# Performance work log

Hardware: AMD Instinct MI355X
Metric: run time of the kernel (lower is better)

The kernel has to match this reference:

```python
import jax, jax.numpy as jnp
import numpy as np

HID = 256; NH = 8; DH = 32; NL = 2
NV = 20000; NT = 50000; NE = 100000; NC = 8; FIN = 64


def setup_inputs() -> dict:
    ks = jax.random.split(jax.random.key(0), 32)
    f = lambda i, sh, s: jax.random.normal(ks[i], sh, dtype=jnp.float32) * s
    return {
        "x_v": f(0, (NV, FIN), 1.0),
        "x_t": f(1, (NT, FIN), 1.0),
        "ei_vt_src": jax.random.randint(ks[2], (NE,), 0, NV),
        "ei_vt_dst": jax.random.randint(ks[3], (NE,), 0, NT),
        "ei_tv_src": jax.random.randint(ks[4], (NE,), 0, NT),
        "ei_tv_dst": jax.random.randint(ks[5], (NE,), 0, NV),
        "ei_tt_src": jax.random.randint(ks[6], (NE,), 0, NT),
        "ei_tt_dst": jax.random.randint(ks[7], (NE,), 0, NT),
        "current": jax.random.randint(ks[8], (NC, 2), 0, NV),
        "W_in_v": f(9, (FIN, HID), 0.05), "b_in_v": jnp.zeros((HID,)),
        "W_in_t": f(10, (FIN, HID), 0.05), "b_in_t": jnp.zeros((HID,)),
        "Wk": f(11, (NL, 2, HID, HID), 0.05), "bk": jnp.zeros((NL, 2, HID)),
        "Wq": f(12, (NL, 2, HID, HID), 0.05), "bq": jnp.zeros((NL, 2, HID)),
        "Wv": f(13, (NL, 2, HID, HID), 0.05), "bv": jnp.zeros((NL, 2, HID)),
        "Wa": f(14, (NL, 2, HID, HID), 0.05), "ba": jnp.zeros((NL, 2, HID)),
        "skip": jnp.zeros((NL, 2)),
        "a_rel": f(15, (NL, 3, NH, DH, DH), 0.1),
        "m_rel": f(16, (NL, 3, NH, DH, DH), 0.1),
        "p_rel": jnp.ones((NL, 3, NH)),
        "Ws1": f(17, (2 * HID, HID), 0.05), "bs1": jnp.zeros((HID,)),
        "Ws2": f(18, (HID, 2), 0.05), "bs2": jnp.zeros((2,)),
    }


def reference(x_v, x_t, ei_vt_src, ei_vt_dst, ei_tv_src, ei_tv_dst,
              ei_tt_src, ei_tt_dst, current,
              W_in_v, b_in_v, W_in_t, b_in_t,
              Wk, bk, Wq, bq, Wv, bv, Wa, ba, skip,
              a_rel, m_rel, p_rel, Ws1, bs1, Ws2, bs2):
    scale = 1.0 / jnp.sqrt(jnp.float32(DH))
    # input projections + relu (lin_dict)
    hv = jax.nn.relu(x_v @ W_in_v + b_in_v)
    ht = jax.nn.relu(x_t @ W_in_t + b_in_t)
    # edge types: (src_type, dst_type, rel_idx, src_idx, dst_idx); 0=vehicle, 1=track
    edges = [(0, 1, 0, ei_vt_src, ei_vt_dst),
             (1, 0, 1, ei_tv_src, ei_tv_dst),
             (1, 1, 2, ei_tt_src, ei_tt_dst)]
    for l in range(NL):
        h = (hv, ht)
        proj = lambda W, b, t: (h[t] @ W[l, t] + b[l, t]).reshape(-1, NH, DH)
        k = (proj(Wk, bk, 0), proj(Wk, bk, 1))
        q = (proj(Wq, bq, 0), proj(Wq, bq, 1))
        v = (proj(Wv, bv, 0), proj(Wv, bv, 1))
        agg = [jnp.zeros((NV, NH, DH), jnp.float32),
               jnp.zeros((NT, NH, DH), jnp.float32)]
        for (st, dt, r, si, di) in edges:
            nd = agg[dt].shape[0]
            ke = jnp.einsum('ehd,hdf->ehf', k[st][si], a_rel[l, r])  # [E,H,D]
            ve = jnp.einsum('ehd,hdf->ehf', v[st][si], m_rel[l, r])  # [E,H,D]
            logit = (q[dt][di] * ke).sum(-1) * p_rel[l, r] * scale    # [E,H]
            m = jax.ops.segment_max(logit, di, num_segments=nd)
            e = jnp.exp(logit - m[di])
            s = jax.ops.segment_sum(e, di, num_segments=nd)
            alpha = e / (s[di] + 1e-16)
            agg[dt] = agg[dt] + jax.ops.segment_sum(alpha[..., None] * ve, di,
                                                    num_segments=nd)
        new = []
        for t in (0, 1):
            o = jax.nn.gelu(agg[t].reshape(-1, HID), approximate=False) @ Wa[l, t] + ba[l, t]
            beta = jax.nn.sigmoid(skip[l, t])
            new.append(beta * o + (1.0 - beta) * h[t])
        hv, ht = new
    # batched Scorer over (current vehicles) x (all tracks); cat([track, vehicle])
    veh = hv[current[:, 0]]                 # [C,HID]
    tpart = ht @ Ws1[:HID]                  # [NT,HID]
    vpart = veh @ Ws1[HID:] + bs1           # [C,HID]
    hmid = jax.nn.relu(tpart[None, :, :] + vpart[:, None, :])  # [C,NT,HID]
    out = hmid @ Ws2 + bs2                  # [C,NT,2]
    return out[..., 0], jax.nn.sigmoid(out[..., 1])
```

## Files before the change

### kernel.cpp

```cpp
#include <hip/hip_runtime.h>
#include <hip/hip_bf16.h>
#include <math.h>

#define HID 256
#define NH 8
#define DH 32
#define NL 2
#define NV 20000
#define NT 50000
#define NE 100000
#define NC 8
#define FIN 64

typedef unsigned short u16;
typedef unsigned int u32;
typedef short s16x8 __attribute__((ext_vector_type(8)));
typedef float f32x4 __attribute__((ext_vector_type(4)));

__device__ __forceinline__ float bf2f(u16 u) { return __uint_as_float(((u32)u) << 16); }
__device__ __forceinline__ u16 f2bf(float f) {
    u32 x = __float_as_uint(f);
    u32 r = ((x >> 16) & 1u) + 0x7fffu;
    return (u16)((x + r) >> 16);
}
__device__ __forceinline__ void up2(u32 u, float& a, float& b) {
    a = __uint_as_float(u << 16);
    b = __uint_as_float(u & 0xffff0000u);
}
__device__ __forceinline__ s16x8 gelu8(s16x8 a) {
    s16x8 r;
#pragma unroll
    for (int i = 0; i < 8; i++) {
        float v = bf2f((u16)a[i]);
        v = 0.5f * v * (1.f + erff(v * 0.70710678118654752f));
        r[i] = (short)f2bf(v);
    }
    return r;
}

__global__ void k_zero_i(int* __restrict__ p, int n) {
    for (int i = blockIdx.x * 256 + threadIdx.x; i < n; i += gridDim.x * 256) p[i] = 0;
}

__global__ void k_hist3(const int* __restrict__ d0, const int* __restrict__ d1, const int* __restrict__ d2,
                        int* __restrict__ cnt3) {
    int r = blockIdx.x >> 9;
    int b = blockIdx.x & 511;
    const int* dst = (r == 0) ? d0 : (r == 1) ? d1 : d2;
    int* cnt = cnt3 + (size_t)r * NT;
    for (int e = b * 256 + threadIdx.x; e < NE; e += 512 * 256)
        atomicAdd(&cnt[dst[e]], 1);
}

__global__ __launch_bounds__(1024) void k_scan3(const int* __restrict__ cnt3,
                                                int* __restrict__ rp0, int* __restrict__ rp1, int* __restrict__ rp2) {
    int r = blockIdx.x;
    const int* cnt = cnt3 + (size_t)r * NT;
    int* rp = (r == 0) ? rp0 : (r == 1) ? rp1 : rp2;
    int n = (r == 1) ? NV : NT;
    __shared__ int wsum[16];
    __shared__ int carry_s;
    int t = threadIdx.x, lane = t & 63, wv = t >> 6;
    if (t == 0) { carry_s = 0; rp[0] = 0; }
    __syncthreads();
    for (int base = 0; base < n; base += 1024) {
        int v = (base + t < n) ? cnt[base + t] : 0;
        int x = v;
#pragma unroll
        for (int off = 1; off < 64; off <<= 1) {
            int y = __shfl_up(x, off, 64);
            if (lane >= off) x += y;
        }
        if (lane == 63) wsum[wv] = x;
        __syncthreads();
        if (wv == 0 && lane < 16) {
            int s = wsum[lane];
#pragma unroll
            for (int off = 1; off < 16; off <<= 1) {
                int y = __shfl_up(s, off, 64);
                if (lane >= off) s += y;
            }
            wsum[lane] = s;
        }
        __syncthreads();
        int prefix = carry_s + (wv > 0 ? wsum[wv - 1] : 0);
        if (base + t < n) rp[base + t + 1] = prefix + x;
        __syncthreads();
        if (t == 0) carry_s += wsum[15];
        __syncthreads();
    }
}

__global__ void k_copy3(const int* __restrict__ rp0, const int* __restrict__ rp1, const int* __restrict__ rp2,
                        int* __restrict__ fill3) {
    int r = blockIdx.x >> 8;
    int b = blockIdx.x & 255;
    const int* rp = (r == 0) ? rp0 : (r == 1) ? rp1 : rp2;
    int n = (r == 1) ? NV : NT;
    int* fill = fill3 + (size_t)r * NT;
    for (int i = b * 256 + threadIdx.x; i < n; i += 256 * 256) fill[i] = rp[i];
}

__global__ void k_scatter3(const int* __restrict__ d0, const int* __restrict__ s0,
                           const int* __restrict__ d1, const int* __restrict__ s1,
                           const int* __restrict__ d2, const int* __restrict__ s2,
                           int* __restrict__ fill3,
                           int* __restrict__ es0, int* __restrict__ es1, int* __restrict__ es2) {
    int r = blockIdx.x >> 9;
    int b = blockIdx.x & 511;
    const int* dst = (r == 0) ? d0 : (r == 1) ? d1 : d2;
    const int* src = (r == 0) ? s0 : (r == 1) ? s1 : s2;
    int* fill = fill3 + (size_t)r * NT;
    int* es = (r == 0) ? es0 : (r == 1) ? es1 : es2;
    for (int e = b * 256 + threadIdx.x; e < NE; e += 512 * 256) {
        int d = dst[e];
        int p = atomicAdd(&fill[d], 1);
        es[p] = src[e];
    }
}

__global__ __launch_bounds__(256) void k_in_proj(const float* __restrict__ X, const float* __restrict__ W,
                          const float* __restrict__ b, u16* __restrict__ Y, int N) {
    const int NPB = 16;
    __shared__ float xs[NPB][FIN];
    int n0 = blockIdx.x * NPB;
    int t = threadIdx.x;
    for (int idx = t; idx < NPB * FIN; idx += 256) {
        int i = idx >> 6, c = idx & 63;
        int n = n0 + i;
        xs[i][c] = (n < N) ? X[(size_t)n * FIN + c] : 0.f;
    }
    __syncthreads();
    float acc[NPB];
#pragma unroll
    for (int i = 0; i < NPB; i++) acc[i] = 0.f;
    for (int c = 0; c < FIN; c++) {
        float w = W[c * HID + t];
#pragma unroll
        for (int i = 0; i < NPB; i++) acc[i] += xs[i][c] * w;
    }
    float bb = b[t];
    for (int i = 0; i < NPB; i++) {
        int n = n0 + i;
        if (n < N) Y[(size_t)n * HID + t] = f2bf(fmaxf(acc[i] + bb, 0.f));
    }
}

__device__ __forceinline__ int swz_idx(int k, int n) {
    int ks = k >> 5, r = k & 31;
    int j = r & 7;
    int l = ((r >> 3) << 4) | (n & 15);
    int nt = n >> 4;
    return ((ks * 16 + nt) * 64 + l) * 8 + j;
}

__global__ __launch_bounds__(256) void k_fuse_w(const float* __restrict__ W, const float* __restrict__ b,
                        const float* __restrict__ R, u16* __restrict__ Wsw, float* __restrict__ bout) {
    int h = blockIdx.x;
    __shared__ float sR[DH * DH];
    int t = threadIdx.x;
    for (int idx = t; idx < DH * DH; idx += 256) sR[idx] = R[h * DH * DH + idx];
    __syncthreads();
    int f = t & 31, c0 = t >> 5;
    for (int c = c0; c < HID; c += 8) {
        float acc = 0.f;
#pragma unroll
        for (int d = 0; d < DH; d++) acc += W[c * HID + h * DH + d] * sR[d * DH + f];
        Wsw[swz_idx(c, h * DH + f)] = f2bf(acc);
    }
    if (t < DH) {
        float acc = 0.f;
#pragma unroll
        for (int d = 0; d < DH; d++) acc += b[h * DH + d] * sR[d * DH + t];
        bout[h * DH + t] = acc;
    }
}

__global__ __launch_bounds__(256) void k_swz_multi(const float* __restrict__ Wq, const float* __restrict__ Wa,
                                                   const float* __restrict__ Ws1, u16* __restrict__ out) {
    int slot = blockIdx.x >> 8;
    int idx = ((blockIdx.x & 255) << 8) | threadIdx.x;
    const float* src = (slot < 4) ? (Wq + (size_t)slot * 65536)
                     : (slot < 8) ? (Wa + (size_t)(slot - 4) * 65536)
                                  : Ws1;
    int j = idx & 7, l = (idx >> 3) & 63, nt = (idx >> 9) & 15, ks = idx >> 13;
    int k = ks * 32 + (l >> 4) * 8 + j;
    int n = nt * 16 + (l & 15);
    out[(size_t)slot * 65536 + idx] = f2bf(src[k * HID + n]);
}

template <int MODE, int GELU>
__global__ __launch_bounds__(256) void k_mm(const u16* __restrict__ X, const u16* __restrict__ Wsw,
                                            const float* __restrict__ bias, void* __restrict__ Y,
                                            const float* __restrict__ skip_, int N) {
    int tid = threadIdx.x;
    int w = tid >> 6, lane = tid & 63;
    int r0 = blockIdx.x * 16;
    int rA = r0 + (lane & 15);
    int koffg = lane >> 4;
    s16x8 a[8];
    if (rA < N) {
        const s16x8* ap = (const s16x8*)(X + (size_t)rA * HID) + koffg;
#pragma unroll
        for (int ks = 0; ks < 8; ks++) a[ks] = ap[ks * 4];
    } else {
#pragma unroll
        for (int ks = 0; ks < 8; ks++) a[ks] = (s16x8){0, 0, 0, 0, 0, 0, 0, 0};
    }
    if (GELU) {
#pragma unroll
        for (int ks = 0; ks < 8; ks++) a[ks] = gelu8(a[ks]);
    }
    f32x4 acc[4];
#pragma unroll
    for (int nt = 0; nt < 4; nt++) acc[nt] = (f32x4){0.f, 0.f, 0.f, 0.f};
    const s16x8* wp = (const s16x8*)Wsw;
#pragma unroll
    for (int ks = 0; ks < 8; ks++) {
        const s16x8* wq = wp + (size_t)ks * 16 * 64 + lane;
#pragma unroll
        for (int nt = 0; nt < 4; nt++) {
            s16x8 b = wq[(w * 4 + nt) * 64];
            acc[nt] = __builtin_amdgcn_mfma_f32_16x16x32_bf16(a[ks], b, acc[nt], 0, 0, 0);
        }
    }
    int colb = lane & 15;
    int rowb = r0 + koffg * 4;
    float beta = 0.f, ombeta = 0.f;
    if (MODE == 2) { beta = 1.f / (1.f + expf(-skip_[0])); ombeta = 1.f - beta; }
#pragma unroll
    for (int nt = 0; nt < 4; nt++) {
        int col = w * 64 + nt * 16 + colb;
        float bb = (MODE == 1 || MODE == 3) ? 0.f : bias[col];
#pragma unroll
        for (int j = 0; j < 4; j++) {
            int row = rowb + j;
            if (row < N) {
                float v = acc[nt][j] + bb;
                if (MODE == 0 || MODE == 3) {
                    ((u16*)Y)[(size_t)row * HID + col] = f2bf(v);
                } else if (MODE == 1) {
                    ((float*)Y)[(size_t)row * HID + col] = v;
                } else {
                    u16* hp = (u16*)Y + (size_t)row * HID + col;
                    *hp = f2bf(beta * v + ombeta * bf2f(*hp));
                }
            }
        }
    }
}

__global__ __launch_bounds__(256) void k_mm2(const u16* __restrict__ X,
                                             const u16* __restrict__ W1, const float* __restrict__ b1, u16* __restrict__ Y1,
                                             const u16* __restrict__ W2, const float* __restrict__ b2, u16* __restrict__ Y2,
                                             int N) {
    int tid = threadIdx.x;
    int w = tid >> 6, lane = tid & 63;
    int r0 = blockIdx.x * 16;
    int rA = r0 + (lane & 15);
    int koffg = lane >> 4;
    s16x8 a[8];
    if (rA < N) {
        const s16x8* ap = (const s16x8*)(X + (size_t)rA * HID) + koffg;
#pragma unroll
        for (int ks = 0; ks < 8; ks++) a[ks] = ap[ks * 4];
    } else {
#pragma unroll
        for (int ks = 0; ks < 8; ks++) a[ks] = (s16x8){0, 0, 0, 0, 0, 0, 0, 0};
    }
    int colb = lane & 15;
    int rowb = r0 + koffg * 4;
#pragma unroll
    for (int pass = 0; pass < 2; pass++) {
        const u16* Wsw = pass ? W2 : W1;
        const float* bias = pass ? b2 : b1;
        u16* Y = pass ? Y2 : Y1;
        f32x4 acc[4];
#pragma unroll
        for (int nt = 0; nt < 4; nt++) acc[nt] = (f32x4){0.f, 0.f, 0.f, 0.f};
        const s16x8* wp = (const s16x8*)Wsw;
#pragma unroll
        for (int ks = 0; ks < 8; ks++) {
            const s16x8* wq = wp + (size_t)ks * 16 * 64 + lane;
#pragma unroll
            for (int nt = 0; nt < 4; nt++) {
                s16x8 b = wq[(w * 4 + nt) * 64];
                acc[nt] = __builtin_amdgcn_mfma_f32_16x16x32_bf16(a[ks], b, acc[nt], 0, 0, 0);
            }
        }
#pragma unroll
        for (int nt = 0; nt < 4; nt++) {
            int col = w * 64 + nt * 16 + colb;
            float bb = bias[col];
#pragma unroll
            for (int j = 0; j < 4; j++) {
                int row = rowb + j;
                if (row < N) Y[(size_t)row * HID + col] = f2bf(acc[nt][j] + bb);
            }
        }
    }
}

__global__ __launch_bounds__(256) void k_mm3(const u16* __restrict__ X,
                                             const u16* __restrict__ W0, const float* __restrict__ b0, u16* __restrict__ Y0,
                                             const u16* __restrict__ W1, const float* __restrict__ b1, u16* __restrict__ Y1,
                                             const u16* __restrict__ W2, const float* __restrict__ b2, u16* __restrict__ Y2,
                                             int N) {
    int tid = threadIdx.x;
    int w = tid >> 6, lane = tid & 63;
    int r0 = blockIdx.x * 16;
    int rA = r0 + (lane & 15);
    int koffg = lane >> 4;
    s16x8 a[8];
    if (rA < N) {
        const s16x8* ap = (const s16x8*)(X + (size_t)rA * HID) + koffg;
#pragma unroll
        for (int ks = 0; ks < 8; ks++) a[ks] = ap[ks * 4];
    } else {
#pragma unroll
        for (int ks = 0; ks < 8; ks++) a[ks] = (s16x8){0, 0, 0, 0, 0, 0, 0, 0};
    }
    int colb = lane & 15;
    int rowb = r0 + koffg * 4;
#pragma unroll
    for (int pass = 0; pass < 3; pass++) {
        const u16* Wsw = (pass == 0) ? W0 : (pass == 1) ? W1 : W2;
        const float* bias = (pass == 0) ? b0 : (pass == 1) ? b1 : b2;
        u16* Y = (pass == 0) ? Y0 : (pass == 1) ? Y1 : Y2;
        f32x4 acc[4];
#pragma unroll
        for (int nt = 0; nt < 4; nt++) acc[nt] = (f32x4){0.f, 0.f, 0.f, 0.f};
        const s16x8* wp = (const s16x8*)Wsw;
#pragma unroll
        for (int ks = 0; ks < 8; ks++) {
            const s16x8* wq = wp + (size_t)ks * 16 * 64 + lane;
#pragma unroll
            for (int nt = 0; nt < 4; nt++) {
                s16x8 b = wq[(w * 4 + nt) * 64];
                acc[nt] = __builtin_amdgcn_mfma_f32_16x16x32_bf16(a[ks], b, acc[nt], 0, 0, 0);
            }
        }
#pragma unroll
        for (int nt = 0; nt < 4; nt++) {
            int col = w * 64 + nt * 16 + colb;
            float bb = bias[col];
#pragma unroll
            for (int j = 0; j < 4; j++) {
                int row = rowb + j;
                if (row < N) Y[(size_t)row * HID + col] = f2bf(acc[nt][j] + bb);
            }
        }
    }
}

__device__ __forceinline__ void attn_pass(const u16* __restrict__ kA, const u16* __restrict__ vM,
                                          const int* __restrict__ es, int jb, int je,
                                          float q0, float q1, float q2, float q3, float ph, int lane4,
                                          float& o0, float& o1, float& o2, float& o3) {
    float m = -INFINITY, ss = 0.f, a0 = 0.f, a1 = 0.f, a2 = 0.f, a3 = 0.f;
    uint2 kuN = {0, 0}, vuN = {0, 0};
    if (jb < je) {
        int s0 = es[jb];
        kuN = *(const uint2*)(kA + (size_t)s0 * HID + lane4);
        vuN = *(const uint2*)(vM + (size_t)s0 * HID + lane4);
    }
    for (int j = jb; j < je; j++) {
        uint2 ku = kuN, vu = vuN;
        if (j + 1 < je) {
            int s1 = es[j + 1];
            kuN = *(const uint2*)(kA + (size_t)s1 * HID + lane4);
            vuN = *(const uint2*)(vM + (size_t)s1 * HID + lane4);
        }
        float k0, k1, k2, k3; up2(ku.x, k0, k1); up2(ku.y, k2, k3);
        float part = q0 * k0 + q1 * k1 + q2 * k2 + q3 * k3;
        part += __shfl_xor(part, 1, 64);
        part += __shfl_xor(part, 2, 64);
        part += __shfl_xor(part, 4, 64);
        float logit = part * ph;
        float nm = fmaxf(m, logit);
        float corr = expf(m - nm);
        float ee = expf(logit - nm);
        float v0, v1, v2, v3; up2(vu.x, v0, v1); up2(vu.y, v2, v3);
        ss = ss * corr + ee;
        a0 = a0 * corr + ee * v0; a1 = a1 * corr + ee * v1;
        a2 = a2 * corr + ee * v2; a3 = a3 * corr + ee * v3;
        m = nm;
    }
    float inv = 1.f / (ss + 1e-16f);
    o0 += a0 * inv; o1 += a1 * inv; o2 += a2 * inv; o3 += a3 * inv;
}

__global__ __launch_bounds__(256) void k_node_attn(
        const u16* __restrict__ q, const u16* __restrict__ kA, const u16* __restrict__ vM,
        const int* __restrict__ rp, const int* __restrict__ es,
        const float* __restrict__ P, float scale,
        u16* __restrict__ agg, int Nd) {
    int node = blockIdx.x * 4 + (threadIdx.x >> 6);
    if (node >= Nd) return;
    int lane = threadIdx.x & 63;
    float ph = P[lane >> 3] * scale;
    uint2 qu = *(const uint2*)(q + (size_t)node * HID + lane * 4);
    float q0, q1, q2, q3; up2(qu.x, q0, q1); up2(qu.y, q2, q3);
    float o0 = 0.f, o1 = 0.f, o2 = 0.f, o3 = 0.f;
    attn_pass(kA, vM, es, rp[node], rp[node + 1], q0, q1, q2, q3, ph, lane * 4, o0, o1, o2, o3);
    u16* ap = agg + (size_t)node * HID + lane * 4;
    ap[0] = f2bf(o0); ap[1] = f2bf(o1); ap[2] = f2bf(o2); ap[3] = f2bf(o3);
}

__global__ __launch_bounds__(256) void k_node_attn2(
        const u16* __restrict__ q,
        const u16* __restrict__ kA0, const u16* __restrict__ vM0,
        const int* __restrict__ rp0, const int* __restrict__ es0, const float* __restrict__ P0,
        const u16* __restrict__ kA1, const u16* __restrict__ vM1,
        const int* __restrict__ rp1, const int* __restrict__ es1, const float* __restrict__ P1,
        float scale, u16* __restrict__ agg, int Nd) {
    int node = blockIdx.x * 4 + (threadIdx.x >> 6);
    if (node >= Nd) return;
    int lane = threadIdx.x & 63;
    int h = lane >> 3;
    float ph0 = P0[h] * scale, ph1 = P1[h] * scale;
    uint2 qu = *(const uint2*)(q + (size_t)node * HID + lane * 4);
    float q0, q1, q2, q3; up2(qu.x, q0, q1); up2(qu.y, q2, q3);
    float o0 = 0.f, o1 = 0.f, o2 = 0.f, o3 = 0.f;
    attn_pass(kA0, vM0, es0, rp0[node], rp0[node + 1], q0, q1, q2, q3, ph0, lane * 4, o0, o1, o2, o3);
    attn_pass(kA1, vM1, es1, rp1[node], rp1[node + 1], q0, q1, q2, q3, ph1, lane * 4, o0, o1, o2, o3);
    u16* ap = agg + (size_t)node * HID + lane * 4;
    ap[0] = f2bf(o0); ap[1] = f2bf(o1); ap[2] = f2bf(o2); ap[3] = f2bf(o3);
}

__global__ void k_vpart(const u16* __restrict__ hv, const int* __restrict__ current,
                        const float* __restrict__ Ws1, const float* __restrict__ bs1,
                        float* __restrict__ vpart) {
    __shared__ float row[HID];
    int t = threadIdx.x;
    for (int c = 0; c < NC; c++) {
        int n = current[c * 2];
        row[t] = bf2f(hv[(size_t)n * HID + t]);
        __syncthreads();
        float acc = 0.f;
        for (int i = 0; i < HID; i++) acc += row[i] * Ws1[(size_t)(HID + i) * HID + t];
        vpart[c * HID + t] = acc + bs1[t];
        __syncthreads();
    }
}

__global__ __launch_bounds__(256) void k_final(const u16* __restrict__ tpart, const float* __restrict__ vpart,
                        const float* __restrict__ Ws2, const float* __restrict__ bs2,
                        float* __restrict__ out) {
    __shared__ float vp[NC * HID];
    int t = threadIdx.x;
    for (int idx = t; idx < NC * HID; idx += 256) vp[idx] = vpart[idx];
    __syncthreads();
    int lane = t & 63, w = t >> 6;
    float w20[4], w21[4];
#pragma unroll
    for (int i = 0; i < 4; i++) {
        w20[i] = Ws2[(lane + 64 * i) * 2 + 0];
        w21[i] = Ws2[(lane + 64 * i) * 2 + 1];
    }
    float b0 = bs2[0], b1 = bs2[1];
    for (int n = blockIdx.x * 4 + w; n < NT; n += gridDim.x * 4) {
        float tp[4];
#pragma unroll
        for (int i = 0; i < 4; i++) tp[i] = bf2f(tpart[(size_t)n * HID + lane + 64 * i]);
#pragma unroll
        for (int c = 0; c < NC; c++) {
            float a0 = 0.f, a1 = 0.f;
#pragma unroll
            for (int i = 0; i < 4; i++) {
                float hm = fmaxf(tp[i] + vp[c * HID + lane + 64 * i], 0.f);
                a0 += hm * w20[i];
                a1 += hm * w21[i];
            }
#pragma unroll
            for (int off = 32; off >= 1; off >>= 1) {
                a0 += __shfl_xor(a0, off, 64);
                a1 += __shfl_xor(a1, off, 64);
            }
            if (lane == 0) {
                out[(size_t)c * NT + n] = a0 + b0;
                float z = a1 + b1;
                out[(size_t)NC * NT + (size_t)c * NT + n] = 1.f / (1.f + expf(-z));
            }
        }
    }
}

extern "C" void kernel_launch(void* const* d_in, const int* in_sizes, int n_in,
                              void* d_out, int out_size, void* d_ws, size_t ws_size,
                              hipStream_t stream) {
    (void)in_sizes; (void)n_in; (void)out_size;
    const float* x_v    = (const float*)d_in[0];
    const float* x_t    = (const float*)d_in[1];
    const int* ei_vt_s  = (const int*)d_in[2];
    const int* ei_vt_d  = (const int*)d_in[3];
    const int* ei_tv_s  = (const int*)d_in[4];
    const int* ei_tv_d  = (const int*)d_in[5];
    const int* ei_tt_s  = (const int*)d_in[6];
    const int* ei_tt_d  = (const int*)d_in[7];
    const int* current  = (const int*)d_in[8];
    const float* W_in_v = (const float*)d_in[9];
    const float* b_in_v = (const float*)d_in[10];
    const float* W_in_t = (const float*)d_in[11];
    const float* b_in_t = (const float*)d_in[12];
    const float* Wk     = (const float*)d_in[13];
    const float* bk     = (const float*)d_in[14];
    const float* Wq     = (const float*)d_in[15];
    const float* bq     = (const float*)d_in[16];
    const float* Wv     = (const float*)d_in[17];
    const float* bv     = (const float*)d_in[18];
    const float* Wa     = (const float*)d_in[19];
    const float* ba     = (const float*)d_in[20];
    const float* skip   = (const float*)d_in[21];
    const float* a_rel  = (const float*)d_in[22];
    const float* m_rel  = (const float*)d_in[23];
    const float* p_rel  = (const float*)d_in[24];
    const float* Ws1    = (const float*)d_in[25];
    const float* bs1    = (const float*)d_in[26];
    const float* Ws2    = (const float*)d_in[27];
    const float* bs2    = (const float*)d_in[28];

    char* p = (char*)d_ws;
    auto alloc = [&](size_t bytes) -> char* {
        char* r = p;
        p += (bytes + 255) & ~(size_t)255;
        return r;
    };
    u16* hv   = (u16*)alloc((size_t)NV * HID * 2);
    u16* ht   = (u16*)alloc((size_t)NT * HID * 2);
    u16* qb   = (u16*)alloc((size_t)NT * HID * 2);
    u16* qv   = (u16*)alloc((size_t)NV * HID * 2);
    u16* kA   = (u16*)alloc((size_t)NT * HID * 2);
    u16* vM   = (u16*)alloc((size_t)NT * HID * 2);
    u16* kA0  = (u16*)alloc((size_t)NV * HID * 2);
    u16* vM0  = (u16*)alloc((size_t)NV * HID * 2);
    u16* agg  = (u16*)alloc((size_t)NT * HID * 2);
    int* rp_vt = (int*)alloc((size_t)(NT + 1) * 4);
    int* rp_tv = (int*)alloc((size_t)(NV + 1) * 4);
    int* rp_tt = (int*)alloc((size_t)(NT + 1) * 4);
    int* es_vt = (int*)alloc((size_t)NE * 4);
    int* es_tv = (int*)alloc((size_t)NE * 4);
    int* es_tt = (int*)alloc((size_t)NE * 4);
    int* cnt3  = (int*)alloc((size_t)3 * NT * 4);
    int* fill3 = (int*)alloc((size_t)3 * NT * 4);
    float* vp  = (float*)alloc((size_t)NC * HID * 4);
    float* bkF = (float*)alloc(HID * 4);
    float* bvF = (float*)alloc(HID * 4);
    u16*  wswK = (u16*)alloc((size_t)HID * HID * 2);
    u16*  wswV = (u16*)alloc((size_t)HID * HID * 2);
    u16*  wswK2 = (u16*)alloc((size_t)HID * HID * 2);
    u16*  wswV2 = (u16*)alloc((size_t)HID * HID * 2);
    float* bkF2 = (float*)alloc(HID * 4);
    float* bvF2 = (float*)alloc(HID * 4);
    u16*  wswA = (u16*)alloc((size_t)9 * HID * HID * 2);
    if ((size_t)(p - (char*)d_ws) > ws_size) return;

    const float scale = 0.17677669529663687f;

    k_zero_i<<<256, 256, 0, stream>>>(cnt3, 3 * NT);
    k_hist3<<<3 * 512, 256, 0, stream>>>(ei_vt_d, ei_tv_d, ei_tt_d, cnt3);
    k_scan3<<<3, 1024, 0, stream>>>(cnt3, rp_vt, rp_tv, rp_tt);
    k_copy3<<<3 * 256, 256, 0, stream>>>(rp_vt, rp_tv, rp_tt, fill3);
    k_scatter3<<<3 * 512, 256, 0, stream>>>(ei_vt_d, ei_vt_s, ei_tv_d, ei_tv_s, ei_tt_d, ei_tt_s,
                                            fill3, es_vt, es_tv, es_tt);

    k_swz_multi<<<9 * 256, 256, 0, stream>>>(Wq, Wa, Ws1, wswA);

    k_in_proj<<<(NV + 15) / 16, 256, 0, stream>>>(x_v, W_in_v, b_in_v, hv, NV);
    k_in_proj<<<(NT + 15) / 16, 256, 0, stream>>>(x_t, W_in_t, b_in_t, ht, NT);

    const int GV = (NV + 15) / 16, GT = (NT + 15) / 16;

    for (int l = 0; l < NL; l++) {
        const float* Wk0 = Wk + (size_t)(l * 2 + 0) * HID * HID;
        const float* Wk1 = Wk + (size_t)(l * 2 + 1) * HID * HID;
        const float* bk0 = bk + (l * 2 + 0) * HID, *bk1 = bk + (l * 2 + 1) * HID;
        const float* Wv0 = Wv + (size_t)(l * 2 + 0) * HID * HID;
        const float* Wv1 = Wv + (size_t)(l * 2 + 1) * HID * HID;
        const float* bv0 = bv + (l * 2 + 0) * HID, *bv1 = bv + (l * 2 + 1) * HID;
        const float* bq0 = bq + (l * 2 + 0) * HID, *bq1 = bq + (l * 2 + 1) * HID;
        const u16* WqS0 = wswA + (size_t)(l * 2 + 0) * 65536;
        const u16* WqS1 = wswA + (size_t)(l * 2 + 1) * 65536;
        const u16* WaS0 = wswA + (size_t)(4 + l * 2 + 0) * 65536;
        const u16* WaS1 = wswA + (size_t)(4 + l * 2 + 1) * 65536;
        const float* A0 = a_rel + (size_t)(l * 3 + 0) * NH * DH * DH;
        const float* A1 = a_rel + (size_t)(l * 3 + 1) * NH * DH * DH;
        const float* A2 = a_rel + (size_t)(l * 3 + 2) * NH * DH * DH;
        const float* M0 = m_rel + (size_t)(l * 3 + 0) * NH * DH * DH;
        const float* M1 = m_rel + (size_t)(l * 3 + 1) * NH * DH * DH;
        const float* M2 = m_rel + (size_t)(l * 3 + 2) * NH * DH * DH;
        const float* P0 = p_rel + (size_t)(l * 3 + 0) * NH;
        const float* P1 = p_rel + (size_t)(l * 3 + 1) * NH;
        const float* P2 = p_rel + (size_t)(l * 3 + 2) * NH;

        k_fuse_w<<<NH, 256, 0, stream>>>(Wk0, bk0, A0, wswK, bkF);
        k_fuse_w<<<NH, 256, 0, stream>>>(Wv0, bv0, M0, wswV, bvF);
        k_mm3<<<GV, 256, 0, stream>>>(hv, WqS0, bq0, qv, wswK, bkF, kA0, wswV, bvF, vM0, NV);

        k_fuse_w<<<NH, 256, 0, stream>>>(Wk1, bk1, A1, wswK, bkF);
        k_fuse_w<<<NH, 256, 0, stream>>>(Wv1, bv1, M1, wswV, bvF);
        k_mm3<<<GT, 256, 0, stream>>>(ht, WqS1, bq1, qb, wswK, bkF, kA, wswV, bvF, vM, NT);

        k_node_attn<<<(NV + 3) / 4, 256, 0, stream>>>(qv, kA, vM, rp_tv, es_tv, P1, scale, agg, NV);

        k_mm<2, 1><<<GV, 256, 0, stream>>>(agg, WaS0, ba + (l * 2 + 0) * HID, hv, skip + (l * 2 + 0), NV);

        k_fuse_w<<<NH, 256, 0, stream>>>(Wk1, bk1, A2, wswK2, bkF2);
        k_fuse_w<<<NH, 256, 0, stream>>>(Wv1, bv1, M2, wswV2, bvF2);
        k_mm2<<<GT, 256, 0, stream>>>(ht, wswK2, bkF2, kA, wswV2, bvF2, vM, NT);

        k_node_attn2<<<(NT + 3) / 4, 256, 0, stream>>>(qb, kA0, vM0, rp_vt, es_vt, P0,
                                                       kA, vM, rp_tt, es_tt, P2, scale, agg, NT);

        k_mm<2, 1><<<GT, 256, 0, stream>>>(agg, WaS1, ba + (l * 2 + 1) * HID, ht, skip + (l * 2 + 1), NT);
    }

    k_vpart<<<1, 256, 0, stream>>>(hv, current, Ws1, bs1, vp);
    u16* tpart = kA;
    k_mm<3, 0><<<GT, 256, 0, stream>>>(ht, wswA + (size_t)8 * 65536, nullptr, (void*)tpart, nullptr, NT);
    k_final<<<2048, 256, 0, stream>>>(tpart, vp, Ws2, bs2, (float*)d_out);
}
```

Baseline: 1.097 ms.

## Fuse final track output GEMM with scorer projection, merge weight-fusion launches

The last layer's track Wa GEMM with skip blend is fused with the Ws1 track projection. The blended tile is kept in shared memory instead of writing ht and re-reading it, which removes a kernel launch and a full pass over the track features. The K and V weight-fusion kernels are merged into one launch per relation. The attention edge loop now prefetches two edges ahead instead of one to hide gather latency, at some register cost.

Result: faster. 989.6 us (-9.8%).

```diff
diff --git a/kernel.cpp b/kernel.cpp
--- a/kernel.cpp
+++ b/kernel.cpp
@@ -154,9 +154,18 @@
     return ((ks * 16 + nt) * 64 + l) * 8 + j;
 }
 
-__global__ __launch_bounds__(256) void k_fuse_w(const float* __restrict__ W, const float* __restrict__ b,
-                        const float* __restrict__ R, u16* __restrict__ Wsw, float* __restrict__ bout) {
-    int h = blockIdx.x;
+__global__ __launch_bounds__(256) void k_fuse_w2(
+        const float* __restrict__ Wk_, const float* __restrict__ bk_, const float* __restrict__ Rk,
+        u16* __restrict__ WswK, float* __restrict__ bkO,
+        const float* __restrict__ Wv_, const float* __restrict__ bv_, const float* __restrict__ Rv,
+        u16* __restrict__ WswV, float* __restrict__ bvO) {
+    int h = blockIdx.x & 7;
+    int which = blockIdx.x >> 3;
+    const float* W = which ? Wv_ : Wk_;
+    const float* b = which ? bv_ : bk_;
+    const float* R = which ? Rv : Rk;
+    u16* Wsw = which ? WswV : WswK;
+    float* bout = which ? bvO : bkO;
     __shared__ float sR[DH * DH];
     int t = threadIdx.x;
     for (int idx = t; idx < DH * DH; idx += 256) sR[idx] = R[h * DH * DH + idx];
@@ -246,6 +255,74 @@
                     *hp = f2bf(beta * v + ombeta * bf2f(*hp));
                 }
             }
+        }
+    }
+}
+
+__global__ __launch_bounds__(256) void k_mm_gt(const u16* __restrict__ agg, const u16* __restrict__ WaSw,
+                                               const float* __restrict__ ba_, const float* __restrict__ skip_,
+                                               const u16* __restrict__ ht_old, const u16* __restrict__ Ws1Sw,
+                                               u16* __restrict__ tpart, int N) {
+    __shared__ u16 sH[16][264];
+    int tid = threadIdx.x;
+    int w = tid >> 6, lane = tid & 63;
+    int r0 = blockIdx.x * 16;
+    int rA = r0 + (lane & 15);
+    int koffg = lane >> 4;
+    s16x8 a[8];
+    {
+        const s16x8* ap = (const s16x8*)(agg + (size_t)rA * HID) + koffg;
+#pragma unroll
+        for (int ks = 0; ks < 8; ks++) a[ks] = gelu8(ap[ks * 4]);
+    }
+    f32x4 acc[4];
+#pragma unroll
+    for (int nt = 0; nt < 4; nt++) acc[nt] = (f32x4){0.f, 0.f, 0.f, 0.f};
+    const s16x8* wp = (const s16x8*)WaSw;
+#pragma unroll
+    for (int ks = 0; ks < 8; ks++) {
+        const s16x8* wq = wp + (size_t)ks * 16 * 64 + lane;
+#pragma unroll
+        for (int nt = 0; nt < 4; nt++)
+            acc[nt] = __builtin_amdgcn_mfma_f32_16x16x32_bf16(a[ks], wq[(w * 4 + nt) * 64], acc[nt], 0, 0, 0);
+    }
+    float beta = 1.f / (1.f + expf(-skip_[0])), ombeta = 1.f - beta;
+    int colb = lane & 15;
+    int rowl = koffg * 4;
+#pragma unroll
+    for (int nt = 0; nt < 4; nt++) {
+        int col = w * 64 + nt * 16 + colb;
+        float bb = ba_[col];
+#pragma unroll
+        for (int j = 0; j < 4; j++) {
+            int row = r0 + rowl + j;
+            float v = acc[nt][j] + bb;
+            float o = beta * v + ombeta * bf2f(ht_old[(size_t)row * HID + col]);
+            sH[rowl + j][col] = f2bf(o);
+        }
+    }
+    __syncthreads();
+    s16x8 a2[8];
+#pragma unroll
+    for (int ks = 0; ks < 8; ks++)
+        a2[ks] = *(const s16x8*)&sH[lane & 15][ks * 32 + koffg * 8];
+#pragma unroll
+    for (int nt = 0; nt < 4; nt++) acc[nt] = (f32x4){0.f, 0.f, 0.f, 0.f};
+    const s16x8* wp2 = (const s16x8*)Ws1Sw;
+#pragma unroll
+    for (int ks = 0; ks < 8; ks++) {
+        const s16x8* wq = wp2 + (size_t)ks * 16 * 64 + lane;
+#pragma unroll
+        for (int nt = 0; nt < 4; nt++)
+            acc[nt] = __builtin_amdgcn_mfma_f32_16x16x32_bf16(a2[ks], wq[(w * 4 + nt) * 64], acc[nt], 0, 0, 0);
+    }
+#pragma unroll
+    for (int nt = 0; nt < 4; nt++) {
+        int col = w * 64 + nt * 16 + colb;
+#pragma unroll
+        for (int j = 0; j < 4; j++) {
+            int row = r0 + rowl + j;
+            if (row < N) tpart[(size_t)row * HID + col] = f2bf(acc[nt][j]);
         }
     }
 }
@@ -358,18 +435,24 @@
                                           float q0, float q1, float q2, float q3, float ph, int lane4,
                                           float& o0, float& o1, float& o2, float& o3) {
     float m = -INFINITY, ss = 0.f, a0 = 0.f, a1 = 0.f, a2 = 0.f, a3 = 0.f;
-    uint2 kuN = {0, 0}, vuN = {0, 0};
+    uint2 ku0 = {0, 0}, vu0 = {0, 0}, ku1 = {0, 0}, vu1 = {0, 0};
     if (jb < je) {
-        int s0 = es[jb];
-        kuN = *(const uint2*)(kA + (size_t)s0 * HID + lane4);
-        vuN = *(const uint2*)(vM + (size_t)s0 * HID + lane4);
+        int s = es[jb];
+        ku0 = *(const uint2*)(kA + (size_t)s * HID + lane4);
+        vu0 = *(const uint2*)(vM + (size_t)s * HID + lane4);
+    }
+    if (jb + 1 < je) {
+        int s = es[jb + 1];
+        ku1 = *(const uint2*)(kA + (size_t)s * HID + lane4);
+        vu1 = *(const uint2*)(vM + (size_t)s * HID + lane4);
     }
     for (int j = jb; j < je; j++) {
-        uint2 ku = kuN, vu = vuN;
-        if (j + 1 < je) {
-            int s1 = es[j + 1];
-            kuN = *(const uint2*)(kA + (size_t)s1 * HID + lane4);
-            vuN = *(const uint2*)(vM + (size_t)s1 * HID + lane4);
+        uint2 ku = ku0, vu = vu0;
+        ku0 = ku1; vu0 = vu1;
+        if (j + 2 < je) {
+            int s = es[j + 2];
+            ku1 = *(const uint2*)(kA + (size_t)s * HID + lane4);
+            vu1 = *(const uint2*)(vM + (size_t)s * HID + lane4);
         }
         float k0, k1, k2, k3; up2(ku.x, k0, k1); up2(ku.y, k2, k3);
         float part = q0 * k0 + q1 * k1 + q2 * k2 + q3 * k3;
@@ -418,13 +501,14 @@
     if (node >= Nd) return;
     int lane = threadIdx.x & 63;
     int h = lane >> 3;
+    int lane4 = lane * 4;
     float ph0 = P0[h] * scale, ph1 = P1[h] * scale;
-    uint2 qu = *(const uint2*)(q + (size_t)node * HID + lane * 4);
+    uint2 qu = *(const uint2*)(q + (size_t)node * HID + lane4);
     float q0, q1, q2, q3; up2(qu.x, q0, q1); up2(qu.y, q2, q3);
     float o0 = 0.f, o1 = 0.f, o2 = 0.f, o3 = 0.f;
-    attn_pass(kA0, vM0, es0, rp0[node], rp0[node + 1], q0, q1, q2, q3, ph0, lane * 4, o0, o1, o2, o3);
-    attn_pass(kA1, vM1, es1, rp1[node], rp1[node + 1], q0, q1, q2, q3, ph1, lane * 4, o0, o1, o2, o3);
-    u16* ap = agg + (size_t)node * HID + lane * 4;
+    attn_pass(kA0, vM0, es0, rp0[node], rp0[node + 1], q0, q1, q2, q3, ph0, lane4, o0, o1, o2, o3);
+    attn_pass(kA1, vM1, es1, rp1[node], rp1[node + 1], q0, q1, q2, q3, ph1, lane4, o0, o1, o2, o3);
+    u16* ap = agg + (size_t)node * HID + lane4;
     ap[0] = f2bf(o0); ap[1] = f2bf(o1); ap[2] = f2bf(o2); ap[3] = f2bf(o3);
 }
 
@@ -593,30 +677,30 @@
         const float* P1 = p_rel + (size_t)(l * 3 + 1) * NH;
         const float* P2 = p_rel + (size_t)(l * 3 + 2) * NH;
 
-        k_fuse_w<<<NH, 256, 0, stream>>>(Wk0, bk0, A0, wswK, bkF);
-        k_fuse_w<<<NH, 256, 0, stream>>>(Wv0, bv0, M0, wswV, bvF);
+        k_fuse_w2<<<2 * NH, 256, 0, stream>>>(Wk0, bk0, A0, wswK, bkF, Wv0, bv0, M0, wswV, bvF);
         k_mm3<<<GV, 256, 0, stream>>>(hv, WqS0, bq0, qv, wswK, bkF, kA0, wswV, bvF, vM0, NV);
 
-        k_fuse_w<<<NH, 256, 0, stream>>>(Wk1, bk1, A1, wswK, bkF);
-        k_fuse_w<<<NH, 256, 0, stream>>>(Wv1, bv1, M1, wswV, bvF);
+        k_fuse_w2<<<2 * NH, 256, 0, stream>>>(Wk1, bk1, A1, wswK, bkF, Wv1, bv1, M1, wswV, bvF);
         k_mm3<<<GT, 256, 0, stream>>>(ht, WqS1, bq1, qb, wswK, bkF, kA, wswV, bvF, vM, NT);
 
         k_node_attn<<<(NV + 3) / 4, 256, 0, stream>>>(qv, kA, vM, rp_tv, es_tv, P1, scale, agg, NV);
 
         k_mm<2, 1><<<GV, 256, 0, stream>>>(agg, WaS0, ba + (l * 2 + 0) * HID, hv, skip + (l * 2 + 0), NV);
 
-        k_fuse_w<<<NH, 256, 0, stream>>>(Wk1, bk1, A2, wswK2, bkF2);
-        k_fuse_w<<<NH, 256, 0, stream>>>(Wv1, bv1, M2, wswV2, bvF2);
+        k_fuse_w2<<<2 * NH, 256, 0, stream>>>(Wk1, bk1, A2, wswK2, bkF2, Wv1, bv1, M2, wswV2, bvF2);
         k_mm2<<<GT, 256, 0, stream>>>(ht, wswK2, bkF2, kA, wswV2, bvF2, vM, NT);
 
         k_node_attn2<<<(NT + 3) / 4, 256, 0, stream>>>(qb, kA0, vM0, rp_vt, es_vt, P0,
                                                        kA, vM, rp_tt, es_tt, P2, scale, agg, NT);
 
-        k_mm<2, 1><<<GT, 256, 0, stream>>>(agg, WaS1, ba + (l * 2 + 1) * HID, ht, skip + (l * 2 + 1), NT);
+        if (l == 0) {
+            k_mm<2, 1><<<GT, 256, 0, stream>>>(agg, WaS1, ba + (l * 2 + 1) * HID, ht, skip + (l * 2 + 1), NT);
+        } else {
+            k_mm_gt<<<GT, 256, 0, stream>>>(agg, WaS1, ba + (l * 2 + 1) * HID, skip + (l * 2 + 1),
+                                            ht, wswA + (size_t)8 * 65536, kA, NT);
+        }
     }
 
     k_vpart<<<1, 256, 0, stream>>>(hv, current, Ws1, bs1, vp);
-    u16* tpart = kA;
-    k_mm<3, 0><<<GT, 256, 0, stream>>>(ht, wswA + (size_t)8 * 65536, nullptr, (void*)tpart, nullptr, NT);
-    k_final<<<2048, 256, 0, stream>>>(tpart, vp, Ws2, bs2, (float*)d_out);
-}
+    k_final<<<2048, 256, 0, stream>>>(kA , vp, Ws2, bs2, (float*)d_out);
+}
```
